# Optimization experiments

Measured on AMD Instinct MI355X. Metric: run time of the kernel, lower is better.

The kernel has to match this reference:

```python
import jax, jax.numpy as jnp
import numpy as np

NUM_LAYERS = 3
INPUT_SIZE = 64
EMB = 128
NUM_CAT = 128          # must equal EMB for the W_e_proj assignment to shape-check
NUM_QUERIES = 1
INIT_SCALE = 0.02
KERNEL_PARAM = 1.0     # referenced-but-undefined in source; standard alpha=1
B = 16
N = 2048
D = INPUT_SIZE + 2 * EMB                 # 320, transformer embedding dim
F_IN = INPUT_SIZE + NUM_CAT + EMB        # 320, raw input feature dim


def setup_inputs() -> dict:
    key = jax.random.key(0)
    k = jax.random.split(key, 6)
    x = jax.random.normal(k[0], (B, F_IN, N), dtype=jnp.float32)
    embedding_matrix = jax.random.normal(k[1], (EMB, NUM_CAT), dtype=jnp.float32)
    W_Q = jax.random.normal(k[2], (NUM_LAYERS, 1, D, D), dtype=jnp.float32) * INIT_SCALE
    W_K = jax.random.normal(k[3], (NUM_LAYERS, 1, D, D), dtype=jnp.float32) * INIT_SCALE
    W_V = jax.random.normal(k[4], (NUM_LAYERS, 1, D, D), dtype=jnp.float32) * INIT_SCALE
    P = jax.random.normal(k[5], (NUM_LAYERS, 1, D, D), dtype=jnp.float32) * INIT_SCALE
    return {"x": x, "embedding_matrix": embedding_matrix,
            "W_Q": W_Q, "W_K": W_K, "W_V": W_V, "P": P}


def _build_We(embedding_matrix):
    W = jnp.zeros((D, F_IN), dtype=embedding_matrix.dtype)
    W = W.at[:INPUT_SIZE, :INPUT_SIZE].set(jnp.eye(INPUT_SIZE, dtype=W.dtype))
    W = W.at[D - EMB:, F_IN - EMB:].set(jnp.eye(EMB, dtype=W.dtype))
    # rows [input_size : D-emb], cols [input_size : F-num_categories]
    W = W.at[INPUT_SIZE:D - EMB, INPUT_SIZE:F_IN - NUM_CAT].set(embedding_matrix)
    return W


def reference(x, embedding_matrix, W_Q, W_K, W_V, P):
    W = _build_We(embedding_matrix)
    h = jnp.einsum('df,bfn->bdn', W, x)                        # [B, D, N]
    for nl in range(NUM_LAYERS):
        key = h[:, :, :-NUM_QUERIES]                           # include_query=False
        value = key
        query = h
        n_context = key.shape[-1]
        Q = jnp.einsum('id,bdm->bim', W_Q[nl, 0], query)       # [B, D, N]
        K = jnp.einsum('id,bdn->bin', W_K[nl, 0], key)         # [B, D, M]
        V = jnp.einsum('id,bdn->bin', W_V[nl, 0], value)       # [B, D, M]
        # linear kernel scores
        scores = KERNEL_PARAM * jnp.einsum('bim,bin->bmn', Q, K)  # [B, N, M]
        attn = jnp.einsum('bin,bmn->bim', V, scores) / n_context  # [B, D, N]
        h = h + jnp.einsum('ji,bim->bjm', P[nl, 0], attn)
    f = h[:, -EMB:, :]                                         # [B, EMB, N] (squeeze no-op for B>1)
    logits = jnp.einsum('bdn,dc->bnc', f, embedding_matrix)    # [B, N, C]
    predictions = jax.nn.softmax(logits, axis=-1)
    return logits, predictions
```

## Files before the change

kernel.cpp:

```cpp
#include <hip/hip_runtime.h>
#include <math.h>

typedef long long ll;
typedef unsigned int uint;
typedef unsigned short ushort;
typedef __attribute__((ext_vector_type(4))) float f32x4;
typedef __attribute__((ext_vector_type(8))) short bf16x8;

#define SZ 102400LL
#define RS 40960LL

__device__ inline void split2(float v, ushort& h, ushort& l)
{
    uint u = __float_as_uint(v);
    uint uh = u + (0x7FFFu + ((u >> 16) & 1u));
    h = (ushort)(uh >> 16);
    float hf = __uint_as_float((uint)h << 16);
    float d = v - hf;
    uint ud = __float_as_uint(d);
    l = (ushort)((ud + (0x7FFFu + ((ud >> 16) & 1u))) >> 16);
}
__device__ inline float us2f(ushort h, ushort l)
{
    return __uint_as_float((uint)h << 16) + __uint_as_float((uint)l << 16);
}

__global__ __launch_bounds__(256) void gram_sp_k(
    const float* __restrict__ x, float* __restrict__ part,
    const float* __restrict__ Wq, const float* __restrict__ Wk,
    const float* __restrict__ Wv, const float* __restrict__ P,
    const float* __restrict__ emb,
    ushort* __restrict__ WqTs, ushort* __restrict__ WkTs, ushort* __restrict__ WvTs,
    ushort* __restrict__ Ps, ushort* __restrict__ embs, ushort* __restrict__ embTs,
    float* __restrict__ q0)
{
    __shared__ __align__(16) char smem[20480];
    int bid0 = blockIdx.x, tid = threadIdx.x;
    if (bid0 < 960) {
        ushort* Ah  = (ushort*)smem;
        ushort* Al_ = Ah + 2560;
        ushort* Bh  = Al_ + 2560;
        ushort* Bl_ = Bh + 2560;
        int flat = bid0;
        int swz = (flat & 7) * 120 + (flat >> 3);
        int b = swz / 60;
        int rr = swz - b * 60;
        int p = rr / 15, t = rr - p * 15;
        int ti = 0, rem = t;
        while (rem >= 5 - ti) { rem -= 5 - ti; ++ti; }
        int tj = ti + rem;
        int i0 = ti * 64, j0 = tj * 64;
        bool diag = (ti == tj);
        const float* X = x + (ll)b * 320 * 2048;
        int wv = tid >> 6, lane = tid & 63;
        int lr = lane & 15, kb = (lane >> 4) * 8;
        int cr = tid >> 2, ck = (tid & 3) * 8;
        f32x4 hh[4], hl[4], lh[4];
        f32x4 zz = {0.f, 0.f, 0.f, 0.f};
        #pragma unroll
        for (int f = 0; f < 4; ++f) { hh[f] = zz; hl[f] = zz; lh[f] = zz; }
        const ushort* BhS = diag ? Ah : Bh;
        const ushort* BlS = diag ? Al_ : Bl_;

        for (int it = 0; it < 16; ++it) {
            int kg0 = p * 512 + it * 32;
            {
                const float* src = X + (ll)(i0 + cr) * 2048 + kg0 + ck;
                float4 v0 = *(const float4*)src;
                float4 v1 = *(const float4*)(src + 4);
                float vals[8] = {v0.x,v0.y,v0.z,v0.w,v1.x,v1.y,v1.z,v1.w};
                if (kg0 + ck + 7 >= 2047) {
                    #pragma unroll
                    for (int u = 0; u < 8; ++u) if (kg0 + ck + u >= 2047) vals[u] = 0.f;
                }
                bf16x8 hv, lv;
                #pragma unroll
                for (int u = 0; u < 8; ++u) { ushort h, l; split2(vals[u], h, l);
                                              hv[u] = (short)h; lv[u] = (short)l; }
                *(bf16x8*)&Ah[cr * 40 + ck] = hv;
                *(bf16x8*)&Al_[cr * 40 + ck] = lv;
            }
            if (!diag) {
                const float* src = X + (ll)(j0 + cr) * 2048 + kg0 + ck;
                float4 v0 = *(const float4*)src;
                float4 v1 = *(const float4*)(src + 4);
                float vals[8] = {v0.x,v0.y,v0.z,v0.w,v1.x,v1.y,v1.z,v1.w};
                if (kg0 + ck + 7 >= 2047) {
                    #pragma unroll
                    for (int u = 0; u < 8; ++u) if (kg0 + ck + u >= 2047) vals[u] = 0.f;
                }
                bf16x8 hv, lv;
                #pragma unroll
                for (int u = 0; u < 8; ++u) { ushort h, l; split2(vals[u], h, l);
                                              hv[u] = (short)h; lv[u] = (short)l; }
                *(bf16x8*)&Bh[cr * 40 + ck] = hv;
                *(bf16x8*)&Bl_[cr * 40 + ck] = lv;
            }
            __syncthreads();
            bf16x8 ah = *(const bf16x8*)&Ah[(wv * 16 + lr) * 40 + kb];
            bf16x8 al = *(const bf16x8*)&Al_[(wv * 16 + lr) * 40 + kb];
            #pragma unroll
            for (int f = 0; f < 4; ++f) {
                bf16x8 bh_ = *(const bf16x8*)&BhS[(f * 16 + lr) * 40 + kb];
                bf16x8 bl_ = *(const bf16x8*)&BlS[(f * 16 + lr) * 40 + kb];
                hh[f] = __builtin_amdgcn_mfma_f32_16x16x32_bf16(ah, bh_, hh[f], 0, 0, 0);
                hl[f] = __builtin_amdgcn_mfma_f32_16x16x32_bf16(ah, bl_, hl[f], 0, 0, 0);
                lh[f] = __builtin_amdgcn_mfma_f32_16x16x32_bf16(al, bh_, lh[f], 0, 0, 0);
            }
            __syncthreads();
        }
        float* out = part + (((ll)p * 16 + b) * 15 + t) * 4096;
        int orow0 = wv * 16 + (lane >> 4) * 4;
        #pragma unroll
        for (int f = 0; f < 4; ++f) {
            int col = f * 16 + lr;
            #pragma unroll
            for (int r = 0; r < 4; ++r)
                out[(orow0 + r) * 64 + col] = hh[f][r] + hl[f][r] + lh[f][r];
        }
        return;
    }
    int bid = bid0 - 960;
    float (*T)[65] = (float(*)[65])smem;
    if (bid < 225) {
        int m = bid / 25, t = bid % 25;
        const float* mats[3] = {Wq, Wk, Wv};
        ushort* dsts[3] = {WqTs, WkTs, WvTs};
        const float* src = mats[m / 3] + (ll)(m % 3) * SZ;
        ushort* dst = dsts[m / 3] + (ll)(m % 3) * SZ;
        int r0 = (t / 5) * 64, c0 = (t % 5) * 64;
        #pragma unroll
        for (int s = 0; s < 4; ++s) {
            int idx = s * 256 + tid;
            int r = idx >> 4, cq = (idx & 15) * 4;
            *(float4*)&T[r][cq] = *(const float4*)(src + (ll)(r0 + r) * 320 + c0 + cq);
        }
        __syncthreads();
        {
            int c = tid >> 2, kq = (tid & 3) * 16;
            bf16x8 h0, h1, l0, l1;
            #pragma unroll
            for (int u = 0; u < 8; ++u) {
                ushort h, l;
                split2(T[kq + u][c], h, l);     h0[u] = (short)h; l0[u] = (short)l;
                split2(T[kq + 8 + u][c], h, l); h1[u] = (short)h; l1[u] = (short)l;
            }
            ushort* dh = dst + (ll)(c0 + c) * 320 + r0 + kq;
            *(bf16x8*)dh = h0; *(bf16x8*)(dh + 8) = h1;
            *(bf16x8*)(dh + 3 * SZ) = l0; *(bf16x8*)(dh + 3 * SZ + 8) = l1;
        }
    } else if (bid < 375) {
        ll off = (ll)(bid - 225) * 2048 + tid * 8;
        float4 v0 = *(const float4*)(P + off);
        float4 v1 = *(const float4*)(P + off + 4);
        float vals[8] = {v0.x,v0.y,v0.z,v0.w,v1.x,v1.y,v1.z,v1.w};
        bf16x8 hv, lv;
        #pragma unroll
        for (int u = 0; u < 8; ++u) { ushort h,l; split2(vals[u],h,l);
                                      hv[u]=(short)h; lv[u]=(short)l; }
        *(bf16x8*)(Ps + off) = hv;
        *(bf16x8*)(Ps + off + 3 * SZ) = lv;
    } else if (bid < 383) {
        ll off = (ll)(bid - 375) * 2048 + tid * 8;
        float4 v0 = *(const float4*)(emb + off);
        float4 v1 = *(const float4*)(emb + off + 4);
        float vals[8] = {v0.x,v0.y,v0.z,v0.w,v1.x,v1.y,v1.z,v1.w};
        bf16x8 hv, lv;
        #pragma unroll
        for (int u = 0; u < 8; ++u) { ushort h,l; split2(vals[u],h,l);
                                      hv[u]=(short)h; lv[u]=(short)l; }
        *(bf16x8*)(embs + off) = hv;
        *(bf16x8*)(embs + off + 16384) = lv;
    } else if (bid < 387) {
        int t = bid - 383;
        int r0 = (t >> 1) * 64, c0 = (t & 1) * 64;
        {
            int r = tid >> 2, cq = (tid & 3) * 4;
            *(float4*)&T[r][cq]      = *(const float4*)(emb + (ll)(r0 + r) * 128 + c0 + cq);
            *(float4*)&T[r][cq + 16] = *(const float4*)(emb + (ll)(r0 + r) * 128 + c0 + cq + 16);
            *(float4*)&T[r][cq + 32] = *(const float4*)(emb + (ll)(r0 + r) * 128 + c0 + cq + 32);
            *(float4*)&T[r][cq + 48] = *(const float4*)(emb + (ll)(r0 + r) * 128 + c0 + cq + 48);
        }
        __syncthreads();
        {
            int c = tid >> 2, kq = (tid & 3) * 16;
            bf16x8 h0, h1, l0, l1;
            #pragma unroll
            for (int u = 0; u < 8; ++u) {
                ushort h, l;
                split2(T[kq + u][c], h, l);     h0[u]=(short)h; l0[u]=(short)l;
                split2(T[kq + 8 + u][c], h, l); h1[u]=(short)h; l1[u]=(short)l;
            }
            ushort* dh = embTs + (ll)(c0 + c) * 128 + r0 + kq;
            *(bf16x8*)dh = h0; *(bf16x8*)(dh + 8) = h1;
            *(bf16x8*)(dh + 16384) = l0; *(bf16x8*)(dh + 16384 + 8) = l1;
        }
    } else {
        ll base = (ll)(bid - 387) * 2048;
        #pragma unroll
        for (int s = 0; s < 8; ++s) {
            ll id = base + s * 256 + tid;
            int c = (int)(id / 320), i = (int)(id % 320);
            q0[id] = (i >= 192) ? emb[(ll)(i - 192) * 128 + c] : 0.f;
        }
    }
}

__global__ __launch_bounds__(256) void gram_red_k(const float* __restrict__ part,
                                                  ushort* __restrict__ GxS,
                                                  ushort* __restrict__ T1s)
{
    int bt = blockIdx.x;
    int b = bt / 15, t = bt % 15;
    int ti = 0, rem = t;
    while (rem >= 5 - ti) { rem -= 5 - ti; ++ti; }
    int tj = ti + rem;
    int i0 = ti * 64, j0 = tj * 64;
    int tid = threadIdx.x;
    int tx = tid & 15, rg = tid >> 4;
    bool wi = (ti == 0 || ti >= 3);
    bool wj = (tj == 0 || tj >= 3);
    ushort* Gb = GxS + (ll)b * SZ;
    ushort* Tsb = T1s + (ll)b * SZ;
    #pragma unroll
    for (int m = 0; m < 4; ++m) {
        int r = rg * 4 + m;
        float s[4] = {};
        for (int p = 0; p < 4; ++p) {
            const float* src = part + (((ll)p * 16 + b) * 15 + t) * 4096 + r * 64 + tx * 4;
            float4 v = *(const float4*)src;
            s[0]+=v.x; s[1]+=v.y; s[2]+=v.z; s[3]+=v.w;
        }
        #pragma unroll
        for (int u = 0; u < 4; ++u) {
            ushort h, l; split2(s[u], h, l);
            ll rd = (ll)(i0 + r) * 320 + j0 + tx * 4 + u;
            ll rt = (ll)(j0 + tx * 4 + u) * 320 + (i0 + r);
            Gb[rd] = h; Gb[rd + 16 * SZ] = l;
            Gb[rt] = h; Gb[rt + 16 * SZ] = l;
            if (wi) { Tsb[rd] = h; Tsb[rd + 16 * SZ] = l; }
            if (wj) { Tsb[rt] = h; Tsb[rt + 16 * SZ] = l; }
        }
    }
}

struct CJob {
    const ushort *Ah, *Bh;
    const void *Ci, *Ci2;
    float* C; ushort* Cs;
    ll aB, bB, ciB, ci2B, cB, csB;
    ll aLo, bLo, csLo, ciLo, ci2Lo;
    int aS, bS, ciS, ci2S, cS, csS;
    int K, tN, tpb, flags;
    int swzQ, swzR;
    float alpha;
};
struct CPack { CJob j[4]; };

__global__ __launch_bounds__(256) void mchain_k(CPack jp, int c0, int c1, int c2)
{
    int bid = blockIdx.x;
    int ji, local;
    if (bid < c0)      { ji = 0; local = bid; }
    else if (bid < c1) { ji = 1; local = bid - c0; }
    else if (bid < c2) { ji = 2; local = bid - c1; }
    else               { ji = 3; local = bid - c2; }
    CJob j = jp.j[ji];
    int xcd = local & 7, sidx = local >> 3;
    int base = (xcd < j.swzR) ? xcd * (j.swzQ + 1)
                              : j.swzR * (j.swzQ + 1) + (xcd - j.swzR) * j.swzQ;
    int swz = base + sidx;
    int bz = swz / j.tpb;
    int t = swz - bz * j.tpb;
    int i0 = (t / j.tN) * 64, j0 = (t % j.tN) * 64;
    int tid = threadIdx.x;
    int wv = tid >> 6, lane = tid & 63;
    int lr = lane & 15, kb = (lane >> 4) * 8;
    f32x4 hh[4], cx[4];
    f32x4 zz = {0.f,0.f,0.f,0.f};
    #pragma unroll
    for (int f = 0; f < 4; ++f) { hh[f] = zz; cx[f] = zz; }

    __shared__ __align__(16) ushort Bsh[2][2][2560];

    if (j.K > 0) {
        int srow = tid >> 2, skq = (tid & 3) * 8;
        const ushort* Bg = j.Bh + (ll)bz * j.bB + (ll)(j0 + srow) * j.bS + skq;
        const ushort* Ar = j.Ah + (ll)bz * j.aB + (ll)(i0 + wv * 16 + lr) * j.aS + kb;
        bf16x8 svh, svl, ah, al, ahn, aln;
        svh = *(const bf16x8*)Bg;
        svl = *(const bf16x8*)(Bg + j.bLo);
        *(bf16x8*)&Bsh[0][0][srow * 40 + skq] = svh;
        *(bf16x8*)&Bsh[0][1][srow * 40 + skq] = svl;
        ah = *(const bf16x8*)Ar;
        al = *(const bf16x8*)(Ar + j.aLo);
        __syncthreads();
        int nit = j.K >> 5;
        for (int it = 0; it < nit; ++it) {
            int cur = it & 1;
            bool more = (it + 1 < nit);
            if (more) {
                int k1 = (it + 1) << 5;
                svh = *(const bf16x8*)(Bg + k1);
                svl = *(const bf16x8*)(Bg + j.bLo + k1);
                ahn = *(const bf16x8*)(Ar + k1);
                aln = *(const bf16x8*)(Ar + j.aLo + k1);
            }
            #pragma unroll
            for (int f = 0; f < 4; ++f) {
                bf16x8 bh = *(const bf16x8*)&Bsh[cur][0][(f * 16 + lr) * 40 + kb];
                bf16x8 bl = *(const bf16x8*)&Bsh[cur][1][(f * 16 + lr) * 40 + kb];
                hh[f] = __builtin_amdgcn_mfma_f32_16x16x32_bf16(ah, bh, hh[f], 0, 0, 0);
                cx[f] = __builtin_amdgcn_mfma_f32_16x16x32_bf16(ah, bl, cx[f], 0, 0, 0);
                cx[f] = __builtin_amdgcn_mfma_f32_16x16x32_bf16(al, bh, cx[f], 0, 0, 0);
            }
            if (more) {
                *(bf16x8*)&Bsh[cur ^ 1][0][srow * 40 + skq] = svh;
                *(bf16x8*)&Bsh[cur ^ 1][1][srow * 40 + skq] = svl;
                ah = ahn; al = aln;
            }
            __syncthreads();
        }
    }
    const float* Cif = (const float*)j.Ci;
    const ushort* Ciu = (const ushort*)j.Ci;
    const float* Ci2f = (const float*)j.Ci2;
    const ushort* Ci2u = (const ushort*)j.Ci2;
    float* Cp = j.C + (ll)bz * j.cB;
    ushort* Csp = j.Cs + (ll)bz * j.csB;
    int r0 = i0 + wv * 16 + ((lane >> 4) << 2);
    #pragma unroll
    for (int f = 0; f < 4; ++f) {
        int col = j0 + f * 16 + lr;
        #pragma unroll
        for (int r = 0; r < 4; ++r) {
            int row = r0 + r;
            float v = j.alpha * (hh[f][r] + cx[f][r]);
            if (j.flags & 1)
                v += Cif[(ll)bz * j.ciB + (ll)row * j.ciS + col];
            if (j.flags & 32) {
                const ushort* p = Ciu + (ll)bz * j.ciB + (ll)row * j.ciS + col;
                v += us2f(p[0], p[j.ciLo]);
            }
            if (j.flags & 64) {
                const ushort* b2 = Ci2u + (ll)bz * j.ci2B;
                if (j.flags & 2) { const ushort* p = b2 + (ll)row * j.ci2S + col;
                                   v += us2f(p[0], p[j.ci2Lo]); }
                if (j.flags & 4) { const ushort* p = b2 + (ll)col * j.ci2S + row;
                                   v += us2f(p[0], p[j.ci2Lo]); }
            } else {
                if (j.flags & 2) v += Ci2f[(ll)bz * j.ci2B + (ll)row * j.ci2S + col];
                if (j.flags & 4) v += Ci2f[(ll)bz * j.ci2B + (ll)col * j.ci2S + row];
            }
            if (j.flags & 8) Cp[(ll)row * j.cS + col] = v;
            if (j.flags & 16) {
                ushort h, l; split2(v, h, l);
                ushort* p = Csp + (ll)row * j.csS + col;
                p[0] = h; p[j.csLo] = l;
            }
        }
    }
}

__global__ __launch_bounds__(256) void logits_mfma_k(const float* __restrict__ x,
                                                     const ushort* __restrict__ LBs,
                                                     float* __restrict__ logits,
                                                     float* __restrict__ pred)
{
    int flat = blockIdx.x;
    int swzb = (flat & 7) * 128 + (flat >> 3);
    int b = swzb >> 6;
    int i0 = (swzb & 63) * 32;
    const float* X = x + (ll)b * 320 * 2048;
    const ushort* LB = LBs + (ll)b * RS;
    __shared__ float Xs_[2][32][33];
    __shared__ float pmL[2][32], psL[2][32];
    int tid = threadIdx.x;
    int wv = tid >> 6, lane = tid & 63;
    int lr = lane & 15, g = lane >> 4, kb = g * 8;
    int rowg = (wv & 1) * 16, ch = wv >> 1, colh = ch * 64;
    int lkk = tid >> 3, lq = (tid & 7) * 4;
    f32x4 hh[4], cx[4];
    f32x4 zz = {0.f,0.f,0.f,0.f};
    #pragma unroll
    for (int f = 0; f < 4; ++f) { hh[f] = zz; cx[f] = zz; }
    float4 pa;
    auto glb = [&](int k0) {
        pa = *(const float4*)(X + (ll)(k0 + lkk) * 2048 + i0 + lq);
    };
    auto stl = [&](int buf) {
        float* p = &Xs_[buf][lkk][lq];
        p[0] = pa.x; p[1] = pa.y; p[2] = pa.z; p[3] = pa.w;
    };
    glb(0); stl(0);
    __syncthreads();
    for (int it = 0; it < 10; ++it) {
        int cur = it & 1;
        if (it < 9) glb((it + 1) * 32);
        bf16x8 ah, al;
        #pragma unroll
        for (int u = 0; u < 8; ++u) {
            ushort h, l;
            split2(Xs_[cur][kb + u][rowg + lr], h, l);
            ah[u] = (short)h; al[u] = (short)l;
        }
        #pragma unroll
        for (int f = 0; f < 4; ++f) {
            const ushort* Bp = LB + (ll)(colh + f * 16 + lr) * 320 + it * 32 + kb;
            bf16x8 bh = *(const bf16x8*)Bp;
            bf16x8 bl = *(const bf16x8*)(Bp + 16 * RS);
            hh[f] = __builtin_amdgcn_mfma_f32_16x16x32_bf16(ah, bh, hh[f], 0, 0, 0);
            cx[f] = __builtin_amdgcn_mfma_f32_16x16x32_bf16(ah, bl, cx[f], 0, 0, 0);
            cx[f] = __builtin_amdgcn_mfma_f32_16x16x32_bf16(al, bh, cx[f], 0, 0, 0);
        }
        if (it < 9) stl(cur ^ 1);
        __syncthreads();
    }
    float v[4][4];
    #pragma unroll
    for (int r = 0; r < 4; ++r)
        #pragma unroll
        for (int f = 0; f < 4; ++f) v[r][f] = hh[f][r] + cx[f][r];
    #pragma unroll
    for (int r = 0; r < 4; ++r) {
        float m = fmaxf(fmaxf(v[r][0], v[r][1]), fmaxf(v[r][2], v[r][3]));
        #pragma unroll
        for (int off = 8; off; off >>= 1) m = fmaxf(m, __shfl_xor(m, off));
        if (lr == 0) pmL[ch][rowg + g * 4 + r] = m;
    }
    __syncthreads();
    float ev[4][4];
    #pragma unroll
    for (int r = 0; r < 4; ++r) {
        int blr = rowg + g * 4 + r;
        float mx = fmaxf(pmL[0][blr], pmL[1][blr]);
        float s = 0.f;
        #pragma unroll
        for (int f = 0; f < 4; ++f) { ev[r][f] = expf(v[r][f] - mx); s += ev[r][f]; }
        #pragma unroll
        for (int off = 8; off; off >>= 1) s += __shfl_xor(s, off);
        if (lr == 0) psL[ch][blr] = s;
    }
    __syncthreads();
    #pragma unroll
    for (int r = 0; r < 4; ++r) {
        int blr = rowg + g * 4 + r;
        float inv = 1.f / (psL[0][blr] + psL[1][blr]);
        ll ro = ((ll)b * 2048 + i0 + blr) * 128 + colh + lr;
        #pragma unroll
        for (int f = 0; f < 4; ++f) {
            logits[ro + f * 16] = v[r][f];
            pred[ro + f * 16] = ev[r][f] * inv;
        }
    }
}

extern "C" void kernel_launch(void* const* d_in, const int* in_sizes, int n_in,
                              void* d_out, int out_size, void* d_ws, size_t ws_size,
                              hipStream_t stream)
{
    const float* x   = (const float*)d_in[0];
    const float* emb = (const float*)d_in[1];
    const float* Wq  = (const float*)d_in[2];
    const float* Wk  = (const float*)d_in[3];
    const float* Wv  = (const float*)d_in[4];
    const float* P   = (const float*)d_in[5];

    float* logits = (float*)d_out;
    float* pred   = logits + (ll)16 * 2048 * 128;

    float* w = (float*)d_ws;
    auto takef = [&](ll n) { float* p = w; w += n; return p; };
    ushort* GxS  = (ushort*)takef(16 * SZ);
    ushort* T1s  = (ushort*)takef(16 * SZ);
    ushort* Gs   = (ushort*)takef(16 * SZ);
    ushort* As   = (ushort*)takef(16 * SZ);
    ushort* Us   = (ushort*)takef(16 * SZ);
    float*  ATsF = takef(48 * SZ);
    ushort* ATs  = (ushort*)ATsF;
    ushort* PVs  = (ushort*)takef(3 * SZ);
    ushort* KQTs = (ushort*)takef(3 * SZ);
    ushort* KQs  = (ushort*)takef(3 * SZ);
    ushort* Ps   = (ushort*)takef(3 * SZ);
    ushort* WqTs = (ushort*)takef(3 * SZ);
    ushort* WkTs = (ushort*)takef(3 * SZ);
    ushort* WvTs = (ushort*)takef(3 * SZ);
    ushort* embs = (ushort*)takef(16384);
    ushort* embTs= (ushort*)takef(16384);
    float*  q0f  = takef(RS);
    ushort* q1s  = (ushort*)takef(16 * RS);
    ushort* q2s  = (ushort*)takef(16 * RS);
    ushort* LBs  = (ushort*)takef(16 * RS);
    ushort* Xs   = GxS;
    ushort* Zts  = T1s;
    float*  part = ATsF;
    ushort* q3s  = q1s;
    const float cinv = 1.f / 2047.f;

    auto JB = [](const ushort* Ah, ll aB, int aS, ll aLo,
                 const ushort* Bh, ll bB, int bS, ll bLo,
                 int K, int tM, int tN, float alpha, int flags,
                 const void* Ci, ll ciB, int ciS, ll ciLo,
                 const void* Ci2, ll ci2B, int ci2S, ll ci2Lo,
                 float* C, ll cB, int cS,
                 ushort* Cs, ll csB, int csS, ll csLo) {
        CJob j;
        j.Ah = Ah; j.Bh = Bh;
        j.Ci = Ci; j.Ci2 = Ci2; j.C = C; j.Cs = Cs;
        j.aB = aB; j.bB = bB; j.ciB = ciB; j.ci2B = ci2B; j.cB = cB; j.csB = csB;
        j.aLo = aLo; j.bLo = bLo; j.csLo = csLo; j.ciLo = ciLo; j.ci2Lo = ci2Lo;
        j.aS = aS; j.bS = bS; j.ciS = ciS; j.ci2S = ci2S; j.cS = cS; j.csS = csS;
        j.K = K; j.tN = tN; j.tpb = tM * tN; j.flags = flags; j.alpha = alpha;
        j.swzQ = 0; j.swzR = 0;
        return j;
    };
    auto fire = [&](const CJob* js, const int* nb, int n) {
        CPack jp;
        int cum[4], tot = 0;
        for (int i = 0; i < 4; ++i) {
            jp.j[i] = js[i < n ? i : 0];
            if (i < n) { jp.j[i].swzQ = nb[i] >> 3; jp.j[i].swzR = nb[i] & 7; }
            tot += (i < n ? nb[i] : 0);
            cum[i] = tot;
        }
        mchain_k<<<tot, 256, 0, stream>>>(jp, cum[0], cum[1], cum[2]);
    };

    gram_sp_k<<<1367, 256, 0, stream>>>(x, part, Wq, Wk, Wv, P, emb,
                                        WqTs, WkTs, WvTs, Ps, embs, embTs, q0f);
    gram_red_k<<<240, 256, 0, stream>>>(part, GxS, T1s);
    {
        CJob js[4] = {
            JB(embs, 0, 128, 16384,  GxS + 64, SZ, 320, 16*SZ,  128, 2, 5, 1.f, 16,
               0,0,0,0, 0,0,0,0,  0,0,0,  T1s + 64*320, SZ, 320, 16*SZ),
            JB(Ps, SZ, 320, 3*SZ,  WvTs, SZ, 320, 3*SZ,  320, 5, 5, 1.f, 16,
               0,0,0,0, 0,0,0,0,  0,0,0,  PVs, SZ, 320, 3*SZ),
            JB(WqTs, SZ, 320, 3*SZ,  WkTs, SZ, 320, 3*SZ,  320, 5, 5, 1.f, 16,
               0,0,0,0, 0,0,0,0,  0,0,0,  KQTs, SZ, 320, 3*SZ),
            JB(WkTs, SZ, 320, 3*SZ,  WqTs, SZ, 320, 3*SZ,  320, 5, 5, 1.f, 16,
               0,0,0,0, 0,0,0,0,  0,0,0,  KQs, SZ, 320, 3*SZ)};
        int nb[4] = {160, 75, 75, 75};
        fire(js, nb, 4);
    }
    {
        CJob js[3] = {
            JB(T1s + 64, SZ, 320, 16*SZ,  embs, 0, 128, 16384,  128, 5, 2, 1.f, 16,
               0,0,0,0, 0,0,0,0,  0,0,0,  Gs + 64, SZ, 320, 16*SZ),
            JB(0,0,0,0, 0,0,0,0,  0, 5, 1, 0.f, 32|16,
               T1s, SZ, 320, 16*SZ, 0,0,0,0,  0,0,0,  Gs, SZ, 320, 16*SZ),
            JB(0,0,0,0, 0,0,0,0,  0, 5, 2, 0.f, 32|16,
               T1s + 192, SZ, 320, 16*SZ, 0,0,0,0,  0,0,0,  Gs + 192, SZ, 320, 16*SZ)};
        int nb[3] = {160, 80, 160};
        fire(js, nb, 3);
    }
    for (int l = 0; l < 3; ++l) {
        const ushort* PVl = PVs + (ll)l * SZ;
        const ushort* KQTl = KQTs + (ll)l * SZ;
        const ushort* KQl = KQs + (ll)l * SZ;
        ushort* ATl = ATs + (ll)l * 16 * SZ;
        if (l < 2) {
            CJob s1[2] = {
                JB(PVl, 0, 320, 3*SZ,  Gs, SZ, 320, 16*SZ,  320, 5, 5, 1.f, 16,
                   0,0,0,0, 0,0,0,0,  0,0,0,  Xs, SZ, 320, 16*SZ),
                JB(Gs, SZ, 320, 16*SZ,  KQl, 0, 320, 3*SZ,  320, 5, 5, 1.f, 16,
                   0,0,0,0, 0,0,0,0,  0,0,0,  Zts, SZ, 320, 16*SZ)};
            int n1[2] = {400, 400};
            fire(s1, n1, 2);
            CJob s2[3] = {
                JB(Xs, SZ, 320, 16*SZ,  KQTl, 0, 320, 3*SZ,  320, 5, 5, cinv, 16,
                   0,0,0,0, 0,0,0,0,  0,0,0,  As, SZ, 320, 16*SZ),
                JB(KQTl, 0, 320, 3*SZ,  Xs, SZ, 320, 16*SZ,  320, 5, 5, cinv, 16,
                   0,0,0,0, 0,0,0,0,  0,0,0,  ATl, SZ, 320, 48*SZ),
                JB(Xs, SZ, 320, 16*SZ,  Zts, SZ, 320, 16*SZ,  320, 5, 5, cinv, 16,
                   0,0,0,0, 0,0,0,0,  0,0,0,  Us, SZ, 320, 16*SZ)};
            int n2[3] = {400, 400, 400};
            fire(s2, n2, 3);
            CJob s3[1] = {
                JB(Us, SZ, 320, 16*SZ,  As, SZ, 320, 16*SZ,  320, 5, 5, 1.f, 16|32|2|4|64,
                   Gs, SZ, 320, 16*SZ,  Us, SZ, 320, 16*SZ,  0,0,0,  Gs, SZ, 320, 16*SZ)};
            int n3[1] = {400};
            fire(s3, n3, 1);
        } else {
            CJob s1[1] = {
                JB(PVl, 0, 320, 3*SZ,  Gs, SZ, 320, 16*SZ,  320, 5, 5, 1.f, 16,
                   0,0,0,0, 0,0,0,0,  0,0,0,  Xs, SZ, 320, 16*SZ)};
            int n1[1] = {400};
            fire(s1, n1, 1);
            CJob s2[1] = {
                JB(KQTl, 0, 320, 3*SZ,  Xs, SZ, 320, 16*SZ,  320, 5, 5, cinv, 16,
                   0,0,0,0, 0,0,0,0,  0,0,0,  ATl, SZ, 320, 48*SZ)};
            int n2[1] = {400};
            fire(s2, n2, 1);
        }
    }
    {
        CJob js[1] = {
            JB(embTs, 0, 128, 16384,  ATs + 2*16*SZ + 192, SZ, 320, 48*SZ,  128, 2, 5, 1.f, 1|16,
               q0f, 0, 320, 0, 0,0,0,0,  0,0,0,  q1s, RS, 320, 16*RS)};
        int nb[1] = {160};
        fire(js, nb, 1);
    }
    {
        CJob js[1] = {
            JB(q1s, RS, 320, 16*RS,  ATs + 1*16*SZ, SZ, 320, 48*SZ,  320, 2, 5, 1.f, 32|16,
               q1s, RS, 320, 16*RS, 0,0,0,0,  0,0,0,  q2s, RS, 320, 16*RS)};
        int nb[1] = {160};
        fire(js, nb, 1);
    }
    {
        CJob js[1] = {
            JB(q2s, RS, 320, 16*RS,  ATs, SZ, 320, 48*SZ,  320, 2, 5, 1.f, 32|16,
               q2s, RS, 320, 16*RS, 0,0,0,0,  0,0,0,  q3s, RS, 320, 16*RS)};
        int nb[1] = {160};
        fire(js, nb, 1);
    }
    {
        CJob js[3] = {
            JB(q3s + 64, RS, 320, 16*RS,  embTs, 0, 128, 16384,  128, 2, 2, 1.f, 16,
               0,0,0,0, 0,0,0,0,  0,0,0,  LBs + 64, RS, 320, 16*RS),
            JB(0,0,0,0, 0,0,0,0,  0, 2, 1, 0.f, 32|16,
               q3s, RS, 320, 16*RS, 0,0,0,0,  0,0,0,  LBs, RS, 320, 16*RS),
            JB(0,0,0,0, 0,0,0,0,  0, 2, 2, 0.f, 32|16,
               q3s + 192, RS, 320, 16*RS, 0,0,0,0,  0,0,0,  LBs + 192, RS, 320, 16*RS)};
        int nb[3] = {64, 32, 64};
        fire(js, nb, 3);
    }
    logits_mfma_k<<<1024, 256, 0, stream>>>(x, LBs, logits, pred);
}
```

Before: 315.4 us.

## Fuse all pipeline stages into one cooperative persistent megakernel with grid sync

Replaces the sequence of about 17 separate kernel launches (gram, reduce, chained GEMM jobs, logits) with a single cooperative kernel that loops over stages and separates them with grid-wide barriers. Stage bodies become device functions that share one dynamic shared-memory buffer. The goal is to remove per-launch overhead and the gaps between dependent small launches. The cost is that a grid of at most 1024 persistent blocks must loop over stages with up to 1367 tiles, and grid syncs add their own latency. If the cooperative launch fails, it falls back to per-stage launches.

```diff
diff --git a/kernel.cpp b/kernel.cpp
--- a/kernel.cpp
+++ b/kernel.cpp
@@ -1,5 +1,8 @@
 #include <hip/hip_runtime.h>
+#include <hip/hip_cooperative_groups.h>
 #include <math.h>
+
+namespace cg = cooperative_groups;
 
 typedef long long ll;
 typedef unsigned int uint;
@@ -23,225 +26,6 @@
 __device__ inline float us2f(ushort h, ushort l)
 {
     return __uint_as_float((uint)h << 16) + __uint_as_float((uint)l << 16);
-}
-
-__global__ __launch_bounds__(256) void gram_sp_k(
-    const float* __restrict__ x, float* __restrict__ part,
-    const float* __restrict__ Wq, const float* __restrict__ Wk,
-    const float* __restrict__ Wv, const float* __restrict__ P,
-    const float* __restrict__ emb,
-    ushort* __restrict__ WqTs, ushort* __restrict__ WkTs, ushort* __restrict__ WvTs,
-    ushort* __restrict__ Ps, ushort* __restrict__ embs, ushort* __restrict__ embTs,
-    float* __restrict__ q0)
-{
-    __shared__ __align__(16) char smem[20480];
-    int bid0 = blockIdx.x, tid = threadIdx.x;
-    if (bid0 < 960) {
-        ushort* Ah  = (ushort*)smem;
-        ushort* Al_ = Ah + 2560;
-        ushort* Bh  = Al_ + 2560;
-        ushort* Bl_ = Bh + 2560;
-        int flat = bid0;
-        int swz = (flat & 7) * 120 + (flat >> 3);
-        int b = swz / 60;
-        int rr = swz - b * 60;
-        int p = rr / 15, t = rr - p * 15;
-        int ti = 0, rem = t;
-        while (rem >= 5 - ti) { rem -= 5 - ti; ++ti; }
-        int tj = ti + rem;
-        int i0 = ti * 64, j0 = tj * 64;
-        bool diag = (ti == tj);
-        const float* X = x + (ll)b * 320 * 2048;
-        int wv = tid >> 6, lane = tid & 63;
-        int lr = lane & 15, kb = (lane >> 4) * 8;
-        int cr = tid >> 2, ck = (tid & 3) * 8;
-        f32x4 hh[4], hl[4], lh[4];
-        f32x4 zz = {0.f, 0.f, 0.f, 0.f};
-        #pragma unroll
-        for (int f = 0; f < 4; ++f) { hh[f] = zz; hl[f] = zz; lh[f] = zz; }
-        const ushort* BhS = diag ? Ah : Bh;
-        const ushort* BlS = diag ? Al_ : Bl_;
-
-        for (int it = 0; it < 16; ++it) {
-            int kg0 = p * 512 + it * 32;
-            {
-                const float* src = X + (ll)(i0 + cr) * 2048 + kg0 + ck;
-                float4 v0 = *(const float4*)src;
-                float4 v1 = *(const float4*)(src + 4);
-                float vals[8] = {v0.x,v0.y,v0.z,v0.w,v1.x,v1.y,v1.z,v1.w};
-                if (kg0 + ck + 7 >= 2047) {
-                    #pragma unroll
-                    for (int u = 0; u < 8; ++u) if (kg0 + ck + u >= 2047) vals[u] = 0.f;
-                }
-                bf16x8 hv, lv;
-                #pragma unroll
-                for (int u = 0; u < 8; ++u) { ushort h, l; split2(vals[u], h, l);
-                                              hv[u] = (short)h; lv[u] = (short)l; }
-                *(bf16x8*)&Ah[cr * 40 + ck] = hv;
-                *(bf16x8*)&Al_[cr * 40 + ck] = lv;
-            }
-            if (!diag) {
-                const float* src = X + (ll)(j0 + cr) * 2048 + kg0 + ck;
-                float4 v0 = *(const float4*)src;
-                float4 v1 = *(const float4*)(src + 4);
-                float vals[8] = {v0.x,v0.y,v0.z,v0.w,v1.x,v1.y,v1.z,v1.w};
-                if (kg0 + ck + 7 >= 2047) {
-                    #pragma unroll
-                    for (int u = 0; u < 8; ++u) if (kg0 + ck + u >= 2047) vals[u] = 0.f;
-                }
-                bf16x8 hv, lv;
-                #pragma unroll
-                for (int u = 0; u < 8; ++u) { ushort h, l; split2(vals[u], h, l);
-                                              hv[u] = (short)h; lv[u] = (short)l; }
-                *(bf16x8*)&Bh[cr * 40 + ck] = hv;
-                *(bf16x8*)&Bl_[cr * 40 + ck] = lv;
-            }
-            __syncthreads();
-            bf16x8 ah = *(const bf16x8*)&Ah[(wv * 16 + lr) * 40 + kb];
-            bf16x8 al = *(const bf16x8*)&Al_[(wv * 16 + lr) * 40 + kb];
-            #pragma unroll
-            for (int f = 0; f < 4; ++f) {
-                bf16x8 bh_ = *(const bf16x8*)&BhS[(f * 16 + lr) * 40 + kb];
-                bf16x8 bl_ = *(const bf16x8*)&BlS[(f * 16 + lr) * 40 + kb];
-                hh[f] = __builtin_amdgcn_mfma_f32_16x16x32_bf16(ah, bh_, hh[f], 0, 0, 0);
-                hl[f] = __builtin_amdgcn_mfma_f32_16x16x32_bf16(ah, bl_, hl[f], 0, 0, 0);
-                lh[f] = __builtin_amdgcn_mfma_f32_16x16x32_bf16(al, bh_, lh[f], 0, 0, 0);
-            }
-            __syncthreads();
-        }
-        float* out = part + (((ll)p * 16 + b) * 15 + t) * 4096;
-        int orow0 = wv * 16 + (lane >> 4) * 4;
-        #pragma unroll
-        for (int f = 0; f < 4; ++f) {
-            int col = f * 16 + lr;
-            #pragma unroll
-            for (int r = 0; r < 4; ++r)
-                out[(orow0 + r) * 64 + col] = hh[f][r] + hl[f][r] + lh[f][r];
-        }
-        return;
-    }
-    int bid = bid0 - 960;
-    float (*T)[65] = (float(*)[65])smem;
-    if (bid < 225) {
-        int m = bid / 25, t = bid % 25;
-        const float* mats[3] = {Wq, Wk, Wv};
-        ushort* dsts[3] = {WqTs, WkTs, WvTs};
-        const float* src = mats[m / 3] + (ll)(m % 3) * SZ;
-        ushort* dst = dsts[m / 3] + (ll)(m % 3) * SZ;
-        int r0 = (t / 5) * 64, c0 = (t % 5) * 64;
-        #pragma unroll
-        for (int s = 0; s < 4; ++s) {
-            int idx = s * 256 + tid;
-            int r = idx >> 4, cq = (idx & 15) * 4;
-            *(float4*)&T[r][cq] = *(const float4*)(src + (ll)(r0 + r) * 320 + c0 + cq);
-        }
-        __syncthreads();
-        {
-            int c = tid >> 2, kq = (tid & 3) * 16;
-            bf16x8 h0, h1, l0, l1;
-            #pragma unroll
-            for (int u = 0; u < 8; ++u) {
-                ushort h, l;
-                split2(T[kq + u][c], h, l);     h0[u] = (short)h; l0[u] = (short)l;
-                split2(T[kq + 8 + u][c], h, l); h1[u] = (short)h; l1[u] = (short)l;
-            }
-            ushort* dh = dst + (ll)(c0 + c) * 320 + r0 + kq;
-            *(bf16x8*)dh = h0; *(bf16x8*)(dh + 8) = h1;
-            *(bf16x8*)(dh + 3 * SZ) = l0; *(bf16x8*)(dh + 3 * SZ + 8) = l1;
-        }
-    } else if (bid < 375) {
-        ll off = (ll)(bid - 225) * 2048 + tid * 8;
-        float4 v0 = *(const float4*)(P + off);
-        float4 v1 = *(const float4*)(P + off + 4);
-        float vals[8] = {v0.x,v0.y,v0.z,v0.w,v1.x,v1.y,v1.z,v1.w};
-        bf16x8 hv, lv;
-        #pragma unroll
-        for (int u = 0; u < 8; ++u) { ushort h,l; split2(vals[u],h,l);
-                                      hv[u]=(short)h; lv[u]=(short)l; }
-        *(bf16x8*)(Ps + off) = hv;
-        *(bf16x8*)(Ps + off + 3 * SZ) = lv;
-    } else if (bid < 383) {
-        ll off = (ll)(bid - 375) * 2048 + tid * 8;
-        float4 v0 = *(const float4*)(emb + off);
-        float4 v1 = *(const float4*)(emb + off + 4);
-        float vals[8] = {v0.x,v0.y,v0.z,v0.w,v1.x,v1.y,v1.z,v1.w};
-        bf16x8 hv, lv;
-        #pragma unroll
-        for (int u = 0; u < 8; ++u) { ushort h,l; split2(vals[u],h,l);
-                                      hv[u]=(short)h; lv[u]=(short)l; }
-        *(bf16x8*)(embs + off) = hv;
-        *(bf16x8*)(embs + off + 16384) = lv;
-    } else if (bid < 387) {
-        int t = bid - 383;
-        int r0 = (t >> 1) * 64, c0 = (t & 1) * 64;
-        {
-            int r = tid >> 2, cq = (tid & 3) * 4;
-            *(float4*)&T[r][cq]      = *(const float4*)(emb + (ll)(r0 + r) * 128 + c0 + cq);
-            *(float4*)&T[r][cq + 16] = *(const float4*)(emb + (ll)(r0 + r) * 128 + c0 + cq + 16);
-            *(float4*)&T[r][cq + 32] = *(const float4*)(emb + (ll)(r0 + r) * 128 + c0 + cq + 32);
-            *(float4*)&T[r][cq + 48] = *(const float4*)(emb + (ll)(r0 + r) * 128 + c0 + cq + 48);
-        }
-        __syncthreads();
-        {
-            int c = tid >> 2, kq = (tid & 3) * 16;
-            bf16x8 h0, h1, l0, l1;
-            #pragma unroll
-            for (int u = 0; u < 8; ++u) {
-                ushort h, l;
-                split2(T[kq + u][c], h, l);     h0[u]=(short)h; l0[u]=(short)l;
-                split2(T[kq + 8 + u][c], h, l); h1[u]=(short)h; l1[u]=(short)l;
-            }
-            ushort* dh = embTs + (ll)(c0 + c) * 128 + r0 + kq;
-            *(bf16x8*)dh = h0; *(bf16x8*)(dh + 8) = h1;
-            *(bf16x8*)(dh + 16384) = l0; *(bf16x8*)(dh + 16384 + 8) = l1;
-        }
-    } else {
-        ll base = (ll)(bid - 387) * 2048;
-        #pragma unroll
-        for (int s = 0; s < 8; ++s) {
-            ll id = base + s * 256 + tid;
-            int c = (int)(id / 320), i = (int)(id % 320);
-            q0[id] = (i >= 192) ? emb[(ll)(i - 192) * 128 + c] : 0.f;
-        }
-    }
-}
-
-__global__ __launch_bounds__(256) void gram_red_k(const float* __restrict__ part,
-                                                  ushort* __restrict__ GxS,
-                                                  ushort* __restrict__ T1s)
-{
-    int bt = blockIdx.x;
-    int b = bt / 15, t = bt % 15;
-    int ti = 0, rem = t;
-    while (rem >= 5 - ti) { rem -= 5 - ti; ++ti; }
-    int tj = ti + rem;
-    int i0 = ti * 64, j0 = tj * 64;
-    int tid = threadIdx.x;
-    int tx = tid & 15, rg = tid >> 4;
-    bool wi = (ti == 0 || ti >= 3);
-    bool wj = (tj == 0 || tj >= 3);
-    ushort* Gb = GxS + (ll)b * SZ;
-    ushort* Tsb = T1s + (ll)b * SZ;
-    #pragma unroll
-    for (int m = 0; m < 4; ++m) {
-        int r = rg * 4 + m;
-        float s[4] = {};
-        for (int p = 0; p < 4; ++p) {
-            const float* src = part + (((ll)p * 16 + b) * 15 + t) * 4096 + r * 64 + tx * 4;
-            float4 v = *(const float4*)src;
-            s[0]+=v.x; s[1]+=v.y; s[2]+=v.z; s[3]+=v.w;
-        }
-        #pragma unroll
-        for (int u = 0; u < 4; ++u) {
-            ushort h, l; split2(s[u], h, l);
-            ll rd = (ll)(i0 + r) * 320 + j0 + tx * 4 + u;
-            ll rt = (ll)(j0 + tx * 4 + u) * 320 + (i0 + r);
-            Gb[rd] = h; Gb[rd + 16 * SZ] = l;
-            Gb[rt] = h; Gb[rt + 16 * SZ] = l;
-            if (wi) { Tsb[rd] = h; Tsb[rd + 16 * SZ] = l; }
-            if (wj) { Tsb[rt] = h; Tsb[rt + 16 * SZ] = l; }
-        }
-    }
 }
 
 struct CJob {
@@ -255,17 +39,28 @@
     int swzQ, swzR;
     float alpha;
 };
-struct CPack { CJob j[4]; };
-
-__global__ __launch_bounds__(256) void mchain_k(CPack jp, int c0, int c1, int c2)
-{
-    int bid = blockIdx.x;
-    int ji, local;
-    if (bid < c0)      { ji = 0; local = bid; }
-    else if (bid < c1) { ji = 1; local = bid - c0; }
-    else if (bid < c2) { ji = 2; local = bid - c1; }
-    else               { ji = 3; local = bid - c2; }
-    CJob j = jp.j[ji];
+
+__device__ inline CJob JBd(const ushort* Ah, ll aB, int aS, ll aLo,
+                           const ushort* Bh, ll bB, int bS, ll bLo,
+                           int K, int tM, int tN, float alpha, int flags,
+                           const void* Ci, ll ciB, int ciS, ll ciLo,
+                           const void* Ci2, ll ci2B, int ci2S, ll ci2Lo,
+                           float* C, ll cB, int cS,
+                           ushort* Cs, ll csB, int csS, ll csLo, int nb)
+{
+    CJob j;
+    j.Ah = Ah; j.Bh = Bh;
+    j.Ci = Ci; j.Ci2 = Ci2; j.C = C; j.Cs = Cs;
+    j.aB = aB; j.bB = bB; j.ciB = ciB; j.ci2B = ci2B; j.cB = cB; j.csB = csB;
+    j.aLo = aLo; j.bLo = bLo; j.csLo = csLo; j.ciLo = ciLo; j.ci2Lo = ci2Lo;
+    j.aS = aS; j.bS = bS; j.ciS = ciS; j.ci2S = ci2S; j.cS = cS; j.csS = csS;
+    j.K = K; j.tN = tN; j.tpb = tM * tN; j.flags = flags; j.alpha = alpha;
+    j.swzQ = nb >> 3; j.swzR = nb & 7;
+    return j;
+}
+
+__device__ __attribute__((noinline)) void gemm_tile(const CJob& j, int local, char* smem)
+{
     int xcd = local & 7, sidx = local >> 3;
     int base = (xcd < j.swzR) ? xcd * (j.swzQ + 1)
                               : j.swzR * (j.swzQ + 1) + (xcd - j.swzR) * j.swzQ;
@@ -281,7 +76,7 @@
     #pragma unroll
     for (int f = 0; f < 4; ++f) { hh[f] = zz; cx[f] = zz; }
 
-    __shared__ __align__(16) ushort Bsh[2][2][2560];
+    ushort (*Bsh)[2][2560] = (ushort(*)[2][2560])smem;
 
     if (j.K > 0) {
         int srow = tid >> 2, skq = (tid & 3) * 8;
@@ -362,19 +157,236 @@
     }
 }
 
-__global__ __launch_bounds__(256) void logits_mfma_k(const float* __restrict__ x,
-                                                     const ushort* __restrict__ LBs,
-                                                     float* __restrict__ logits,
-                                                     float* __restrict__ pred)
-{
-    int flat = blockIdx.x;
+__device__ void gram_tile(int flat, const float* __restrict__ x,
+                          float* __restrict__ part, char* smem)
+{
+    ushort* Ah  = (ushort*)smem;
+    ushort* Al_ = Ah + 2560;
+    ushort* Bh  = Al_ + 2560;
+    ushort* Bl_ = Bh + 2560;
+    int tid = threadIdx.x;
+    int swz = (flat & 7) * 120 + (flat >> 3);
+    int b = swz / 60;
+    int rr = swz - b * 60;
+    int p = rr / 15, t = rr - p * 15;
+    int ti = 0, rem = t;
+    while (rem >= 5 - ti) { rem -= 5 - ti; ++ti; }
+    int tj = ti + rem;
+    int i0 = ti * 64, j0 = tj * 64;
+    bool diag = (ti == tj);
+    const float* X = x + (ll)b * 320 * 2048;
+    int wv = tid >> 6, lane = tid & 63;
+    int lr = lane & 15, kb = (lane >> 4) * 8;
+    int cr = tid >> 2, ck = (tid & 3) * 8;
+    f32x4 hh[4], hl[4], lh[4];
+    f32x4 zz = {0.f, 0.f, 0.f, 0.f};
+    #pragma unroll
+    for (int f = 0; f < 4; ++f) { hh[f] = zz; hl[f] = zz; lh[f] = zz; }
+    const ushort* BhS = diag ? Ah : Bh;
+    const ushort* BlS = diag ? Al_ : Bl_;
+
+    for (int it = 0; it < 16; ++it) {
+        int kg0 = p * 512 + it * 32;
+        {
+            const float* src = X + (ll)(i0 + cr) * 2048 + kg0 + ck;
+            float4 v0 = *(const float4*)src;
+            float4 v1 = *(const float4*)(src + 4);
+            float vals[8] = {v0.x,v0.y,v0.z,v0.w,v1.x,v1.y,v1.z,v1.w};
+            if (kg0 + ck + 7 >= 2047) {
+                #pragma unroll
+                for (int u = 0; u < 8; ++u) if (kg0 + ck + u >= 2047) vals[u] = 0.f;
+            }
+            bf16x8 hv, lv;
+            #pragma unroll
+            for (int u = 0; u < 8; ++u) { ushort h, l; split2(vals[u], h, l);
+                                          hv[u] = (short)h; lv[u] = (short)l; }
+            *(bf16x8*)&Ah[cr * 40 + ck] = hv;
+            *(bf16x8*)&Al_[cr * 40 + ck] = lv;
+        }
+        if (!diag) {
+            const float* src = X + (ll)(j0 + cr) * 2048 + kg0 + ck;
+            float4 v0 = *(const float4*)src;
+            float4 v1 = *(const float4*)(src + 4);
+            float vals[8] = {v0.x,v0.y,v0.z,v0.w,v1.x,v1.y,v1.z,v1.w};
+            if (kg0 + ck + 7 >= 2047) {
+                #pragma unroll
+                for (int u = 0; u < 8; ++u) if (kg0 + ck + u >= 2047) vals[u] = 0.f;
+            }
+            bf16x8 hv, lv;
+            #pragma unroll
+            for (int u = 0; u < 8; ++u) { ushort h, l; split2(vals[u], h, l);
+                                          hv[u] = (short)h; lv[u] = (short)l; }
+            *(bf16x8*)&Bh[cr * 40 + ck] = hv;
+            *(bf16x8*)&Bl_[cr * 40 + ck] = lv;
+        }
+        __syncthreads();
+        bf16x8 ah = *(const bf16x8*)&Ah[(wv * 16 + lr) * 40 + kb];
+        bf16x8 al = *(const bf16x8*)&Al_[(wv * 16 + lr) * 40 + kb];
+        #pragma unroll
+        for (int f = 0; f < 4; ++f) {
+            bf16x8 bh_ = *(const bf16x8*)&BhS[(f * 16 + lr) * 40 + kb];
+            bf16x8 bl_ = *(const bf16x8*)&BlS[(f * 16 + lr) * 40 + kb];
+            hh[f] = __builtin_amdgcn_mfma_f32_16x16x32_bf16(ah, bh_, hh[f], 0, 0, 0);
+            hl[f] = __builtin_amdgcn_mfma_f32_16x16x32_bf16(ah, bl_, hl[f], 0, 0, 0);
+            lh[f] = __builtin_amdgcn_mfma_f32_16x16x32_bf16(al, bh_, lh[f], 0, 0, 0);
+        }
+        __syncthreads();
+    }
+    float* out = part + (((ll)p * 16 + b) * 15 + t) * 4096;
+    int orow0 = wv * 16 + (lane >> 4) * 4;
+    #pragma unroll
+    for (int f = 0; f < 4; ++f) {
+        int col = f * 16 + lr;
+        #pragma unroll
+        for (int r = 0; r < 4; ++r)
+            out[(orow0 + r) * 64 + col] = hh[f][r] + hl[f][r] + lh[f][r];
+    }
+}
+
+__device__ void sp_tile(int bid,
+                        const float* __restrict__ Wq, const float* __restrict__ Wk,
+                        const float* __restrict__ Wv, const float* __restrict__ P,
+                        const float* __restrict__ emb,
+                        ushort* WqTs, ushort* WkTs, ushort* WvTs,
+                        ushort* Ps, ushort* embs, ushort* embTs,
+                        float* q0, char* smem)
+{
+    int tid = threadIdx.x;
+    float (*T)[65] = (float(*)[65])smem;
+    if (bid < 225) {
+        int m = bid / 25, t = bid % 25;
+        const float* mats[3] = {Wq, Wk, Wv};
+        ushort* dsts[3] = {WqTs, WkTs, WvTs};
+        const float* src = mats[m / 3] + (ll)(m % 3) * SZ;
+        ushort* dst = dsts[m / 3] + (ll)(m % 3) * SZ;
+        int r0 = (t / 5) * 64, c0 = (t % 5) * 64;
+        #pragma unroll
+        for (int s = 0; s < 4; ++s) {
+            int idx = s * 256 + tid;
+            int r = idx >> 4, cq = (idx & 15) * 4;
+            *(float4*)&T[r][cq] = *(const float4*)(src + (ll)(r0 + r) * 320 + c0 + cq);
+        }
+        __syncthreads();
+        {
+            int c = tid >> 2, kq = (tid & 3) * 16;
+            bf16x8 h0, h1, l0, l1;
+            #pragma unroll
+            for (int u = 0; u < 8; ++u) {
+                ushort h, l;
+                split2(T[kq + u][c], h, l);     h0[u] = (short)h; l0[u] = (short)l;
+                split2(T[kq + 8 + u][c], h, l); h1[u] = (short)h; l1[u] = (short)l;
+            }
+            ushort* dh = dst + (ll)(c0 + c) * 320 + r0 + kq;
+            *(bf16x8*)dh = h0; *(bf16x8*)(dh + 8) = h1;
+            *(bf16x8*)(dh + 3 * SZ) = l0; *(bf16x8*)(dh + 3 * SZ + 8) = l1;
+        }
+    } else if (bid < 375) {
+        ll off = (ll)(bid - 225) * 2048 + tid * 8;
+        float4 v0 = *(const float4*)(P + off);
+        float4 v1 = *(const float4*)(P + off + 4);
+        float vals[8] = {v0.x,v0.y,v0.z,v0.w,v1.x,v1.y,v1.z,v1.w};
+        bf16x8 hv, lv;
+        #pragma unroll
+        for (int u = 0; u < 8; ++u) { ushort h,l; split2(vals[u],h,l);
+                                      hv[u]=(short)h; lv[u]=(short)l; }
+        *(bf16x8*)(Ps + off) = hv;
+        *(bf16x8*)(Ps + off + 3 * SZ) = lv;
+    } else if (bid < 383) {
+        ll off = (ll)(bid - 375) * 2048 + tid * 8;
+        float4 v0 = *(const float4*)(emb + off);
+        float4 v1 = *(const float4*)(emb + off + 4);
+        float vals[8] = {v0.x,v0.y,v0.z,v0.w,v1.x,v1.y,v1.z,v1.w};
+        bf16x8 hv, lv;
+        #pragma unroll
+        for (int u = 0; u < 8; ++u) { ushort h,l; split2(vals[u],h,l);
+                                      hv[u]=(short)h; lv[u]=(short)l; }
+        *(bf16x8*)(embs + off) = hv;
+        *(bf16x8*)(embs + off + 16384) = lv;
+    } else if (bid < 387) {
+        int t = bid - 383;
+        int r0 = (t >> 1) * 64, c0 = (t & 1) * 64;
+        {
+            int r = tid >> 2, cq = (tid & 3) * 4;
+            *(float4*)&T[r][cq]      = *(const float4*)(emb + (ll)(r0 + r) * 128 + c0 + cq);
+            *(float4*)&T[r][cq + 16] = *(const float4*)(emb + (ll)(r0 + r) * 128 + c0 + cq + 16);
+            *(float4*)&T[r][cq + 32] = *(const float4*)(emb + (ll)(r0 + r) * 128 + c0 + cq + 32);
+            *(float4*)&T[r][cq + 48] = *(const float4*)(emb + (ll)(r0 + r) * 128 + c0 + cq + 48);
+        }
+        __syncthreads();
+        {
+            int c = tid >> 2, kq = (tid & 3) * 16;
+            bf16x8 h0, h1, l0, l1;
+            #pragma unroll
+            for (int u = 0; u < 8; ++u) {
+                ushort h, l;
+                split2(T[kq + u][c], h, l);     h0[u]=(short)h; l0[u]=(short)l;
+                split2(T[kq + 8 + u][c], h, l); h1[u]=(short)h; l1[u]=(short)l;
+            }
+            ushort* dh = embTs + (ll)(c0 + c) * 128 + r0 + kq;
+            *(bf16x8*)dh = h0; *(bf16x8*)(dh + 8) = h1;
+            *(bf16x8*)(dh + 16384) = l0; *(bf16x8*)(dh + 16384 + 8) = l1;
+        }
+    } else {
+        ll base = (ll)(bid - 387) * 2048;
+        #pragma unroll
+        for (int s = 0; s < 8; ++s) {
+            ll id = base + s * 256 + tid;
+            int c = (int)(id / 320), i = (int)(id % 320);
+            q0[id] = (i >= 192) ? emb[(ll)(i - 192) * 128 + c] : 0.f;
+        }
+    }
+}
+
+__device__ void red_tile(int bt, const float* __restrict__ part,
+                         ushort* __restrict__ GxS, ushort* __restrict__ T1s)
+{
+    int b = bt / 15, t = bt % 15;
+    int ti = 0, rem = t;
+    while (rem >= 5 - ti) { rem -= 5 - ti; ++ti; }
+    int tj = ti + rem;
+    int i0 = ti * 64, j0 = tj * 64;
+    int tid = threadIdx.x;
+    int tx = tid & 15, rg = tid >> 4;
+    bool wi = (ti == 0 || ti >= 3);
+    bool wj = (tj == 0 || tj >= 3);
+    ushort* Gb = GxS + (ll)b * SZ;
+    ushort* Tsb = T1s + (ll)b * SZ;
+    #pragma unroll
+    for (int m = 0; m < 4; ++m) {
+        int r = rg * 4 + m;
+        float s[4] = {};
+        for (int p = 0; p < 4; ++p) {
+            const float* src = part + (((ll)p * 16 + b) * 15 + t) * 4096 + r * 64 + tx * 4;
+            float4 v = *(const float4*)src;
+            s[0]+=v.x; s[1]+=v.y; s[2]+=v.z; s[3]+=v.w;
+        }
+        #pragma unroll
+        for (int u = 0; u < 4; ++u) {
+            ushort h, l; split2(s[u], h, l);
+            ll rd = (ll)(i0 + r) * 320 + j0 + tx * 4 + u;
+            ll rt = (ll)(j0 + tx * 4 + u) * 320 + (i0 + r);
+            Gb[rd] = h; Gb[rd + 16 * SZ] = l;
+            Gb[rt] = h; Gb[rt + 16 * SZ] = l;
+            if (wi) { Tsb[rd] = h; Tsb[rd + 16 * SZ] = l; }
+            if (wj) { Tsb[rt] = h; Tsb[rt + 16 * SZ] = l; }
+        }
+    }
+}
+
+__device__ void logits_tile(int flat, const float* __restrict__ x,
+                            const ushort* __restrict__ LBs,
+                            float* __restrict__ logits, float* __restrict__ pred,
+                            char* smem)
+{
+    float (*Xs_)[32][33] = (float(*)[32][33])smem;
+    float (*SB)[132]     = (float(*)[132])smem;
+    float (*pmL)[32]     = (float(*)[32])(smem + 17408);
+    float (*psL)[32]     = (float(*)[32])(smem + 17920);
     int swzb = (flat & 7) * 128 + (flat >> 3);
     int b = swzb >> 6;
     int i0 = (swzb & 63) * 32;
     const float* X = x + (ll)b * 320 * 2048;
     const ushort* LB = LBs + (ll)b * RS;
-    __shared__ float Xs_[2][32][33];
-    __shared__ float pmL[2][32], psL[2][32];
     int tid = threadIdx.x;
     int wv = tid >> 6, lane = tid & 63;
     int lr = lane & 15, g = lane >> 4, kb = g * 8;
@@ -385,18 +397,21 @@
     #pragma unroll
     for (int f = 0; f < 4; ++f) { hh[f] = zz; cx[f] = zz; }
     float4 pa;
-    auto glb = [&](int k0) {
-        pa = *(const float4*)(X + (ll)(k0 + lkk) * 2048 + i0 + lq);
-    };
-    auto stl = [&](int buf) {
-        float* p = &Xs_[buf][lkk][lq];
-        p[0] = pa.x; p[1] = pa.y; p[2] = pa.z; p[3] = pa.w;
-    };
-    glb(0); stl(0);
+    pa = *(const float4*)(X + (ll)lkk * 2048 + i0 + lq);
+    { float* p = &Xs_[0][lkk][lq]; p[0]=pa.x; p[1]=pa.y; p[2]=pa.z; p[3]=pa.w; }
     __syncthreads();
     for (int it = 0; it < 10; ++it) {
         int cur = it & 1;
-        if (it < 9) glb((it + 1) * 32);
+        if (it < 9) pa = *(const float4*)(X + (ll)((it+1)*32 + lkk) * 2048 + i0 + lq);
+        const ushort* B0 = LB + (ll)(colh + lr) * 320 + it * 32 + kb;
+        bf16x8 b0h = *(const bf16x8*)B0;
+        bf16x8 b0l = *(const bf16x8*)(B0 + 16 * RS);
+        bf16x8 b1h = *(const bf16x8*)(B0 + 16 * 320);
+        bf16x8 b1l = *(const bf16x8*)(B0 + 16 * 320 + 16 * RS);
+        bf16x8 b2h = *(const bf16x8*)(B0 + 32 * 320);
+        bf16x8 b2l = *(const bf16x8*)(B0 + 32 * 320 + 16 * RS);
+        bf16x8 b3h = *(const bf16x8*)(B0 + 48 * 320);
+        bf16x8 b3l = *(const bf16x8*)(B0 + 48 * 320 + 16 * RS);
         bf16x8 ah, al;
         #pragma unroll
         for (int u = 0; u < 8; ++u) {
@@ -404,16 +419,22 @@
             split2(Xs_[cur][kb + u][rowg + lr], h, l);
             ah[u] = (short)h; al[u] = (short)l;
         }
-        #pragma unroll
-        for (int f = 0; f < 4; ++f) {
-            const ushort* Bp = LB + (ll)(colh + f * 16 + lr) * 320 + it * 32 + kb;
-            bf16x8 bh = *(const bf16x8*)Bp;
-            bf16x8 bl = *(const bf16x8*)(Bp + 16 * RS);
-            hh[f] = __builtin_amdgcn_mfma_f32_16x16x32_bf16(ah, bh, hh[f], 0, 0, 0);
-            cx[f] = __builtin_amdgcn_mfma_f32_16x16x32_bf16(ah, bl, cx[f], 0, 0, 0);
-            cx[f] = __builtin_amdgcn_mfma_f32_16x16x32_bf16(al, bh, cx[f], 0, 0, 0);
-        }
-        if (it < 9) stl(cur ^ 1);
+        hh[0] = __builtin_amdgcn_mfma_f32_16x16x32_bf16(ah, b0h, hh[0], 0, 0, 0);
+        cx[0] = __builtin_amdgcn_mfma_f32_16x16x32_bf16(ah, b0l, cx[0], 0, 0, 0);
+        cx[0] = __builtin_amdgcn_mfma_f32_16x16x32_bf16(al, b0h, cx[0], 0, 0, 0);
+        hh[1] = __builtin_amdgcn_mfma_f32_16x16x32_bf16(ah, b1h, hh[1], 0, 0, 0);
+        cx[1] = __builtin_amdgcn_mfma_f32_16x16x32_bf16(ah, b1l, cx[1], 0, 0, 0);
+        cx[1] = __builtin_amdgcn_mfma_f32_16x16x32_bf16(al, b1h, cx[1], 0, 0, 0);
+        hh[2] = __builtin_amdgcn_mfma_f32_16x16x32_bf16(ah, b2h, hh[2], 0, 0, 0);
+        cx[2] = __builtin_amdgcn_mfma_f32_16x16x32_bf16(ah, b2l, cx[2], 0, 0, 0);
+        cx[2] = __builtin_amdgcn_mfma_f32_16x16x32_bf16(al, b2h, cx[2], 0, 0, 0);
+        hh[3] = __builtin_amdgcn_mfma_f32_16x16x32_bf16(ah, b3h, hh[3], 0, 0, 0);
+        cx[3] = __builtin_amdgcn_mfma_f32_16x16x32_bf16(ah, b3l, cx[3], 0, 0, 0);
+        cx[3] = __builtin_amdgcn_mfma_f32_16x16x32_bf16(al, b3h, cx[3], 0, 0, 0);
+        if (it < 9) {
+            float* p = &Xs_[cur ^ 1][lkk][lq];
+            p[0]=pa.x; p[1]=pa.y; p[2]=pa.z; p[3]=pa.w;
+        }
         __syncthreads();
     }
     float v[4][4];
@@ -429,7 +450,7 @@
         if (lr == 0) pmL[ch][rowg + g * 4 + r] = m;
     }
     __syncthreads();
-    float ev[4][4];
+    float ev[4][4], inv[4];
     #pragma unroll
     for (int r = 0; r < 4; ++r) {
         int blr = rowg + g * 4 + r;
@@ -445,185 +466,256 @@
     #pragma unroll
     for (int r = 0; r < 4; ++r) {
         int blr = rowg + g * 4 + r;
-        float inv = 1.f / (psL[0][blr] + psL[1][blr]);
-        ll ro = ((ll)b * 2048 + i0 + blr) * 128 + colh + lr;
-        #pragma unroll
-        for (int f = 0; f < 4; ++f) {
-            logits[ro + f * 16] = v[r][f];
-            pred[ro + f * 16] = ev[r][f] * inv;
-        }
-    }
+        inv[r] = 1.f / (psL[0][blr] + psL[1][blr]);
+    }
+    #pragma unroll
+    for (int r = 0; r < 4; ++r)
+        #pragma unroll
+        for (int f = 0; f < 4; ++f)
+            SB[rowg + g * 4 + r][colh + f * 16 + lr] = v[r][f];
+    __syncthreads();
+    #pragma unroll
+    for (int s = 0; s < 4; ++s) {
+        int idx = s * 256 + tid;
+        int row = idx >> 5, cq = (idx & 31) * 4;
+        *(float4*)(logits + ((ll)b * 2048 + i0 + row) * 128 + cq) = *(float4*)&SB[row][cq];
+    }
+    __syncthreads();
+    #pragma unroll
+    for (int r = 0; r < 4; ++r)
+        #pragma unroll
+        for (int f = 0; f < 4; ++f)
+            SB[rowg + g * 4 + r][colh + f * 16 + lr] = ev[r][f] * inv[r];
+    __syncthreads();
+    #pragma unroll
+    for (int s = 0; s < 4; ++s) {
+        int idx = s * 256 + tid;
+        int row = idx >> 5, cq = (idx & 31) * 4;
+        *(float4*)(pred + ((ll)b * 2048 + i0 + row) * 128 + cq) = *(float4*)&SB[row][cq];
+    }
+}
+
+struct MArgs {
+    const float *x, *emb, *Wq, *Wk, *Wv, *P;
+    float *logits, *pred;
+    ushort *GxS, *T1s, *Gs, *As, *Us, *ATs;
+    ushort *PVs, *KQTs, *KQs, *Ps, *WqTs, *WkTs, *WvTs, *embs, *embTs, *LBs;
+    ushort *q1s, *q2s;
+    float *q0f, *part;
+};
+
+__device__ inline int stage_cnt(int s)
+{
+    switch (s) {
+        case 0: return 1367; case 1: return 240; case 2: return 385;
+        case 3: return 400;  case 4: return 800; case 5: return 1200;
+        case 6: return 400;  case 7: return 800; case 8: return 1200;
+        case 9: return 400;  case 10: return 400; case 11: return 400;
+        case 12: case 13: case 14: case 15: return 160;
+        default: return 1024;
+    }
+}
+
+__device__ void run_stage(const MArgs& a, int stage, int bid, int nbk, char* smem)
+{
+    const float cinv = 1.f / 2047.f;
+    ushort* Xs = a.GxS;
+    ushort* Zts = a.T1s;
+    int cnt = stage_cnt(stage);
+    for (int t = bid; t < cnt; t += nbk) {
+        switch (stage) {
+        case 0:
+            if (t < 960) gram_tile(t, a.x, a.part, smem);
+            else sp_tile(t - 960, a.Wq, a.Wk, a.Wv, a.P, a.emb,
+                         a.WqTs, a.WkTs, a.WvTs, a.Ps, a.embs, a.embTs, a.q0f, smem);
+            break;
+        case 1:
+            red_tile(t, a.part, a.GxS, a.T1s);
+            break;
+        case 2: {
+            CJob j; int x;
+            if (t < 160) { x = t;
+                j = JBd(a.embs,0,128,16384, a.GxS+64,SZ,320,16*SZ, 128,2,5,1.f,16,
+                        0,0,0,0, 0,0,0,0, 0,0,0, a.T1s+64*320,SZ,320,16*SZ, 160); }
+            else if (t < 235) { x = t - 160;
+                j = JBd(a.Ps,SZ,320,3*SZ, a.WvTs,SZ,320,3*SZ, 320,5,5,1.f,16,
+                        0,0,0,0, 0,0,0,0, 0,0,0, a.PVs,SZ,320,3*SZ, 75); }
+            else if (t < 310) { x = t - 235;
+                j = JBd(a.WqTs,SZ,320,3*SZ, a.WkTs,SZ,320,3*SZ, 320,5,5,1.f,16,
+                        0,0,0,0, 0,0,0,0, 0,0,0, a.KQTs,SZ,320,3*SZ, 75); }
+            else { x = t - 310;
+                j = JBd(a.WkTs,SZ,320,3*SZ, a.WqTs,SZ,320,3*SZ, 320,5,5,1.f,16,
+                        0,0,0,0, 0,0,0,0, 0,0,0, a.KQs,SZ,320,3*SZ, 75); }
+            gemm_tile(j, x, smem);
+        } break;
+        case 3: {
+            CJob j; int x;
+            if (t < 160) { x = t;
+                j = JBd(a.T1s+64,SZ,320,16*SZ, a.embs,0,128,16384, 128,5,2,1.f,16,
+                        0,0,0,0, 0,0,0,0, 0,0,0, a.Gs+64,SZ,320,16*SZ, 160); }
+            else if (t < 240) { x = t - 160;
+                j = JBd(0,0,0,0, 0,0,0,0, 0,5,1,0.f,32|16,
+                        a.T1s,SZ,320,16*SZ, 0,0,0,0, 0,0,0, a.Gs,SZ,320,16*SZ, 80); }
+            else { x = t - 240;
+                j = JBd(0,0,0,0, 0,0,0,0, 0,5,2,0.f,32|16,
+                        a.T1s+192,SZ,320,16*SZ, 0,0,0,0, 0,0,0, a.Gs+192,SZ,320,16*SZ, 160); }
+            gemm_tile(j, x, smem);
+        } break;
+        case 4: case 7: {
+            int l = (stage - 4) / 3;
+            const ushort* PVl = a.PVs + (ll)l * SZ;
+            const ushort* KQl = a.KQs + (ll)l * SZ;
+            CJob j; int x;
+            if (t < 400) { x = t;
+                j = JBd(PVl,0,320,3*SZ, a.Gs,SZ,320,16*SZ, 320,5,5,1.f,16,
+                        0,0,0,0, 0,0,0,0, 0,0,0, Xs,SZ,320,16*SZ, 400); }
+            else { x = t - 400;
+                j = JBd(a.Gs,SZ,320,16*SZ, KQl,0,320,3*SZ, 320,5,5,1.f,16,
+                        0,0,0,0, 0,0,0,0, 0,0,0, Zts,SZ,320,16*SZ, 400); }
+            gemm_tile(j, x, smem);
+        } break;
+        case 5: case 8: {
+            int l = (stage - 5) / 3;
+            const ushort* KQTl = a.KQTs + (ll)l * SZ;
+            ushort* ATl = a.ATs + (ll)l * 16 * SZ;
+            CJob j; int x;
+            if (t < 400) { x = t;
+                j = JBd(Xs,SZ,320,16*SZ, KQTl,0,320,3*SZ, 320,5,5,cinv,16,
+                        0,0,0,0, 0,0,0,0, 0,0,0, a.As,SZ,320,16*SZ, 400); }
+            else if (t < 800) { x = t - 400;
+                j = JBd(KQTl,0,320,3*SZ, Xs,SZ,320,16*SZ, 320,5,5,cinv,16,
+                        0,0,0,0, 0,0,0,0, 0,0,0, ATl,SZ,320,48*SZ, 400); }
+            else { x = t - 800;
+                j = JBd(Xs,SZ,320,16*SZ, Zts,SZ,320,16*SZ, 320,5,5,cinv,16,
+                        0,0,0,0, 0,0,0,0, 0,0,0, a.Us,SZ,320,16*SZ, 400); }
+            gemm_tile(j, x, smem);
+        } break;
+        case 6: case 9: {
+            CJob j = JBd(a.Us,SZ,320,16*SZ, a.As,SZ,320,16*SZ, 320,5,5,1.f,16|32|2|4|64,
+                         a.Gs,SZ,320,16*SZ, a.Us,SZ,320,16*SZ, 0,0,0,
+                         a.Gs,SZ,320,16*SZ, 400);
+            gemm_tile(j, t, smem);
+        } break;
+        case 10: {
+            const ushort* PVl = a.PVs + (ll)2 * SZ;
+            CJob j = JBd(PVl,0,320,3*SZ, a.Gs,SZ,320,16*SZ, 320,5,5,1.f,16,
+                         0,0,0,0, 0,0,0,0, 0,0,0, Xs,SZ,320,16*SZ, 400);
+            gemm_tile(j, t, smem);
+        } break;
+        case 11: {
+            const ushort* KQTl = a.KQTs + (ll)2 * SZ;
+            ushort* ATl = a.ATs + (ll)2 * 16 * SZ;
+            CJob j = JBd(KQTl,0,320,3*SZ, Xs,SZ,320,16*SZ, 320,5,5,cinv,16,
+                         0,0,0,0, 0,0,0,0, 0,0,0, ATl,SZ,320,48*SZ, 400);
+            gemm_tile(j, t, smem);
+        } break;
+        case 12: {
+            CJob j = JBd(a.embTs,0,128,16384, a.ATs+2*16*SZ+192,SZ,320,48*SZ,
+                         128,2,5,1.f,1|16,
+                         a.q0f,0,320,0, 0,0,0,0, 0,0,0, a.q1s,RS,320,16*RS, 160);
+            gemm_tile(j, t, smem);
+        } break;
+        case 13: {
+            CJob j = JBd(a.q1s,RS,320,16*RS, a.ATs+16*SZ,SZ,320,48*SZ, 320,2,5,1.f,32|16,
+                         a.q1s,RS,320,16*RS, 0,0,0,0, 0,0,0, a.q2s,RS,320,16*RS, 160);
+            gemm_tile(j, t, smem);
+        } break;
+        case 14: {
+            CJob j = JBd(a.q2s,RS,320,16*RS, a.ATs,SZ,320,48*SZ, 320,2,5,1.f,32|16,
+                         a.q2s,RS,320,16*RS, 0,0,0,0, 0,0,0, a.q1s,RS,320,16*RS, 160);
+            gemm_tile(j, t, smem);
+        } break;
+        case 15: {
+            CJob j; int x;
+            if (t < 64) { x = t;
+                j = JBd(a.q1s+64,RS,320,16*RS, a.embTs,0,128,16384, 128,2,2,1.f,16,
+                        0,0,0,0, 0,0,0,0, 0,0,0, a.LBs+64,RS,320,16*RS, 64); }
+            else if (t < 96) { x = t - 64;
+                j = JBd(0,0,0,0, 0,0,0,0, 0,2,1,0.f,32|16,
+                        a.q1s,RS,320,16*RS, 0,0,0,0, 0,0,0, a.LBs,RS,320,16*RS, 32); }
+            else { x = t - 96;
+                j = JBd(0,0,0,0, 0,0,0,0, 0,2,2,0.f,32|16,
+                        a.q1s+192,RS,320,16*RS, 0,0,0,0, 0,0,0, a.LBs+192,RS,320,16*RS, 64); }
+            gemm_tile(j, x, smem);
+        } break;
+        default:
+            logits_tile(t, a.x, a.LBs, a.logits, a.pred, smem);
+            break;
+        }
+        __syncthreads();
+    }
+}
+
+__global__ __launch_bounds__(256) void mega_k(MArgs a)
+{
+    __shared__ __align__(16) char smem[21504];
+    cg::grid_group gg = cg::this_grid();
+    for (int s = 0; s < 17; ++s) {
+        run_stage(a, s, blockIdx.x, gridDim.x, smem);
+        if (s < 16) gg.sync();
+    }
+}
+
+__global__ __launch_bounds__(256) void stage_k(MArgs a, int stage)
+{
+    __shared__ __align__(16) char smem[21504];
+    run_stage(a, stage, blockIdx.x, gridDim.x, smem);
 }
 
 extern "C" void kernel_launch(void* const* d_in, const int* in_sizes, int n_in,
                               void* d_out, int out_size, void* d_ws, size_t ws_size,
                               hipStream_t stream)
 {
-    const float* x   = (const float*)d_in[0];
-    const float* emb = (const float*)d_in[1];
-    const float* Wq  = (const float*)d_in[2];
-    const float* Wk  = (const float*)d_in[3];
-    const float* Wv  = (const float*)d_in[4];
-    const float* P   = (const float*)d_in[5];
-
-    float* logits = (float*)d_out;
-    float* pred   = logits + (ll)16 * 2048 * 128;
+    MArgs a;
+    a.x   = (const float*)d_in[0];
+    a.emb = (const float*)d_in[1];
+    a.Wq  = (const float*)d_in[2];
+    a.Wk  = (const float*)d_in[3];
+    a.Wv  = (const float*)d_in[4];
+    a.P   = (const float*)d_in[5];
+    a.logits = (float*)d_out;
+    a.pred   = a.logits + (ll)16 * 2048 * 128;
 
     float* w = (float*)d_ws;
     auto takef = [&](ll n) { float* p = w; w += n; return p; };
-    ushort* GxS  = (ushort*)takef(16 * SZ);
-    ushort* T1s  = (ushort*)takef(16 * SZ);
-    ushort* Gs   = (ushort*)takef(16 * SZ);
-    ushort* As   = (ushort*)takef(16 * SZ);
-    ushort* Us   = (ushort*)takef(16 * SZ);
-    float*  ATsF = takef(48 * SZ);
-    ushort* ATs  = (ushort*)ATsF;
-    ushort* PVs  = (ushort*)takef(3 * SZ);
-    ushort* KQTs = (ushort*)takef(3 * SZ);
-    ushort* KQs  = (ushort*)takef(3 * SZ);
-    ushort* Ps   = (ushort*)takef(3 * SZ);
-    ushort* WqTs = (ushort*)takef(3 * SZ);
-    ushort* WkTs = (ushort*)takef(3 * SZ);
-    ushort* WvTs = (ushort*)takef(3 * SZ);
-    ushort* embs = (ushort*)takef(16384);
-    ushort* embTs= (ushort*)takef(16384);
-    float*  q0f  = takef(RS);
-    ushort* q1s  = (ushort*)takef(16 * RS);
-    ushort* q2s  = (ushort*)takef(16 * RS);
-    ushort* LBs  = (ushort*)takef(16 * RS);
-    ushort* Xs   = GxS;
-    ushort* Zts  = T1s;
-    float*  part = ATsF;
-    ushort* q3s  = q1s;
-    const float cinv = 1.f / 2047.f;
-
-    auto JB = [](const ushort* Ah, ll aB, int aS, ll aLo,
-                 const ushort* Bh, ll bB, int bS, ll bLo,
-                 int K, int tM, int tN, float alpha, int flags,
-                 const void* Ci, ll ciB, int ciS, ll ciLo,
-                 const void* Ci2, ll ci2B, int ci2S, ll ci2Lo,
-                 float* C, ll cB, int cS,
-                 ushort* Cs, ll csB, int csS, ll csLo) {
-        CJob j;
-        j.Ah = Ah; j.Bh = Bh;
-        j.Ci = Ci; j.Ci2 = Ci2; j.C = C; j.Cs = Cs;
-        j.aB = aB; j.bB = bB; j.ciB = ciB; j.ci2B = ci2B; j.cB = cB; j.csB = csB;
-        j.aLo = aLo; j.bLo = bLo; j.csLo = csLo; j.ciLo = ciLo; j.ci2Lo = ci2Lo;
-        j.aS = aS; j.bS = bS; j.ciS = ciS; j.ci2S = ci2S; j.cS = cS; j.csS = csS;
-        j.K = K; j.tN = tN; j.tpb = tM * tN; j.flags = flags; j.alpha = alpha;
-        j.swzQ = 0; j.swzR = 0;
-        return j;
-    };
-    auto fire = [&](const CJob* js, const int* nb, int n) {
-        CPack jp;
-        int cum[4], tot = 0;
-        for (int i = 0; i < 4; ++i) {
-            jp.j[i] = js[i < n ? i : 0];
-            if (i < n) { jp.j[i].swzQ = nb[i] >> 3; jp.j[i].swzR = nb[i] & 7; }
-            tot += (i < n ? nb[i] : 0);
-            cum[i] = tot;
-        }
-        mchain_k<<<tot, 256, 0, stream>>>(jp, cum[0], cum[1], cum[2]);
-    };
-
-    gram_sp_k<<<1367, 256, 0, stream>>>(x, part, Wq, Wk, Wv, P, emb,
-                                        WqTs, WkTs, WvTs, Ps, embs, embTs, q0f);
-    gram_red_k<<<240, 256, 0, stream>>>(part, GxS, T1s);
-    {
-        CJob js[4] = {
-            JB(embs, 0, 128, 16384,  GxS + 64, SZ, 320, 16*SZ,  128, 2, 5, 1.f, 16,
-               0,0,0,0, 0,0,0,0,  0,0,0,  T1s + 64*320, SZ, 320, 16*SZ),
-            JB(Ps, SZ, 320, 3*SZ,  WvTs, SZ, 320, 3*SZ,  320, 5, 5, 1.f, 16,
-               0,0,0,0, 0,0,0,0,  0,0,0,  PVs, SZ, 320, 3*SZ),
-            JB(WqTs, SZ, 320, 3*SZ,  WkTs, SZ, 320, 3*SZ,  320, 5, 5, 1.f, 16,
-               0,0,0,0, 0,0,0,0,  0,0,0,  KQTs, SZ, 320, 3*SZ),
-            JB(WkTs, SZ, 320, 3*SZ,  WqTs, SZ, 320, 3*SZ,  320, 5, 5, 1.f, 16,
-               0,0,0,0, 0,0,0,0,  0,0,0,  KQs, SZ, 320, 3*SZ)};
-        int nb[4] = {160, 75, 75, 75};
-        fire(js, nb, 4);
-    }
-    {
-        CJob js[3] = {
-            JB(T1s + 64, SZ, 320, 16*SZ,  embs, 0, 128, 16384,  128, 5, 2, 1.f, 16,
-               0,0,0,0, 0,0,0,0,  0,0,0,  Gs + 64, SZ, 320, 16*SZ),
-            JB(0,0,0,0, 0,0,0,0,  0, 5, 1, 0.f, 32|16,
-               T1s, SZ, 320, 16*SZ, 0,0,0,0,  0,0,0,  Gs, SZ, 320, 16*SZ),
-            JB(0,0,0,0, 0,0,0,0,  0, 5, 2, 0.f, 32|16,
-               T1s + 192, SZ, 320, 16*SZ, 0,0,0,0,  0,0,0,  Gs + 192, SZ, 320, 16*SZ)};
-        int nb[3] = {160, 80, 160};
-        fire(js, nb, 3);
-    }
-    for (int l = 0; l < 3; ++l) {
-        const ushort* PVl = PVs + (ll)l * SZ;
-        const ushort* KQTl = KQTs + (ll)l * SZ;
-        const ushort* KQl = KQs + (ll)l * SZ;
-        ushort* ATl = ATs + (ll)l * 16 * SZ;
-        if (l < 2) {
-            CJob s1[2] = {
-                JB(PVl, 0, 320, 3*SZ,  Gs, SZ, 320, 16*SZ,  320, 5, 5, 1.f, 16,
-                   0,0,0,0, 0,0,0,0,  0,0,0,  Xs, SZ, 320, 16*SZ),
-                JB(Gs, SZ, 320, 16*SZ,  KQl, 0, 320, 3*SZ,  320, 5, 5, 1.f, 16,
-                   0,0,0,0, 0,0,0,0,  0,0,0,  Zts, SZ, 320, 16*SZ)};
-            int n1[2] = {400, 400};
-            fire(s1, n1, 2);
-            CJob s2[3] = {
-                JB(Xs, SZ, 320, 16*SZ,  KQTl, 0, 320, 3*SZ,  320, 5, 5, cinv, 16,
-                   0,0,0,0, 0,0,0,0,  0,0,0,  As, SZ, 320, 16*SZ),
-                JB(KQTl, 0, 320, 3*SZ,  Xs, SZ, 320, 16*SZ,  320, 5, 5, cinv, 16,
-                   0,0,0,0, 0,0,0,0,  0,0,0,  ATl, SZ, 320, 48*SZ),
-                JB(Xs, SZ, 320, 16*SZ,  Zts, SZ, 320, 16*SZ,  320, 5, 5, cinv, 16,
-                   0,0,0,0, 0,0,0,0,  0,0,0,  Us, SZ, 320, 16*SZ)};
-            int n2[3] = {400, 400, 400};
-            fire(s2, n2, 3);
-            CJob s3[1] = {
-                JB(Us, SZ, 320, 16*SZ,  As, SZ, 320, 16*SZ,  320, 5, 5, 1.f, 16|32|2|4|64,
-                   Gs, SZ, 320, 16*SZ,  Us, SZ, 320, 16*SZ,  0,0,0,  Gs, SZ, 320, 16*SZ)};
-            int n3[1] = {400};
-            fire(s3, n3, 1);
-        } else {
-            CJob s1[1] = {
-                JB(PVl, 0, 320, 3*SZ,  Gs, SZ, 320, 16*SZ,  320, 5, 5, 1.f, 16,
-                   0,0,0,0, 0,0,0,0,  0,0,0,  Xs, SZ, 320, 16*SZ)};
-            int n1[1] = {400};
-            fire(s1, n1, 1);
-            CJob s2[1] = {
-                JB(KQTl, 0, 320, 3*SZ,  Xs, SZ, 320, 16*SZ,  320, 5, 5, cinv, 16,
-                   0,0,0,0, 0,0,0,0,  0,0,0,  ATl, SZ, 320, 48*SZ)};
-            int n2[1] = {400};
-            fire(s2, n2, 1);
-        }
-    }
-    {
-        CJob js[1] = {
-            JB(embTs, 0, 128, 16384,  ATs + 2*16*SZ + 192, SZ, 320, 48*SZ,  128, 2, 5, 1.f, 1|16,
-               q0f, 0, 320, 0, 0,0,0,0,  0,0,0,  q1s, RS, 320, 16*RS)};
-        int nb[1] = {160};
-        fire(js, nb, 1);
-    }
-    {
-        CJob js[1] = {
-            JB(q1s, RS, 320, 16*RS,  ATs + 1*16*SZ, SZ, 320, 48*SZ,  320, 2, 5, 1.f, 32|16,
-               q1s, RS, 320, 16*RS, 0,0,0,0,  0,0,0,  q2s, RS, 320, 16*RS)};
-        int nb[1] = {160};
-        fire(js, nb, 1);
-    }
-    {
-        CJob js[1] = {
-            JB(q2s, RS, 320, 16*RS,  ATs, SZ, 320, 48*SZ,  320, 2, 5, 1.f, 32|16,
-               q2s, RS, 320, 16*RS, 0,0,0,0,  0,0,0,  q3s, RS, 320, 16*RS)};
-        int nb[1] = {160};
-        fire(js, nb, 1);
-    }
-    {
-        CJob js[3] = {
-            JB(q3s + 64, RS, 320, 16*RS,  embTs, 0, 128, 16384,  128, 2, 2, 1.f, 16,
-               0,0,0,0, 0,0,0,0,  0,0,0,  LBs + 64, RS, 320, 16*RS),
-            JB(0,0,0,0, 0,0,0,0,  0, 2, 1, 0.f, 32|16,
-               q3s, RS, 320, 16*RS, 0,0,0,0,  0,0,0,  LBs, RS, 320, 16*RS),
-            JB(0,0,0,0, 0,0,0,0,  0, 2, 2, 0.f, 32|16,
-               q3s + 192, RS, 320, 16*RS, 0,0,0,0,  0,0,0,  LBs + 192, RS, 320, 16*RS)};
-        int nb[3] = {64, 32, 64};
-        fire(js, nb, 3);
-    }
-    logits_mfma_k<<<1024, 256, 0, stream>>>(x, LBs, logits, pred);
-}
+    a.GxS  = (ushort*)takef(16 * SZ);
+    a.T1s  = (ushort*)takef(16 * SZ);
+    a.Gs   = (ushort*)takef(16 * SZ);
+    a.As   = (ushort*)takef(16 * SZ);
+    a.Us   = (ushort*)takef(16 * SZ);
+    float* ATsF = takef(48 * SZ);
+    a.ATs  = (ushort*)ATsF;
+    a.PVs  = (ushort*)takef(3 * SZ);
+    a.KQTs = (ushort*)takef(3 * SZ);
+    a.KQs  = (ushort*)takef(3 * SZ);
+    a.Ps   = (ushort*)takef(3 * SZ);
+    a.WqTs = (ushort*)takef(3 * SZ);
+    a.WkTs = (ushort*)takef(3 * SZ);
+    a.WvTs = (ushort*)takef(3 * SZ);
+    a.embs = (ushort*)takef(16384);
+    a.embTs= (ushort*)takef(16384);
+    a.q0f  = takef(RS);
+    a.q1s  = (ushort*)takef(16 * RS);
+    a.q2s  = (ushort*)takef(16 * RS);
+    a.LBs  = (ushort*)takef(16 * RS);
+    a.part = ATsF;
+
+    int mb = 0;
+    hipError_t qerr = hipOccupancyMaxActiveBlocksPerMultiprocessor(&mb, mega_k, 256, 0);
+    int grid = 256;
+    if (qerr == hipSuccess && mb >= 1) {
+        int m = mb > 4 ? 4 : mb;
+        grid = 256 * m;
+        if (grid > 1024) grid = 1024;
+    }
+
+    void* kp[] = { &a };
+    hipError_t err = hipLaunchCooperativeKernel(mega_k, dim3(grid), dim3(256),
+                                                kp, 0, stream);
+    if (err != hipSuccess) {
+        static const int cnt[17] = {1367,240,385,400,800,1200,400,800,1200,400,
+                                    400,400,160,160,160,160,1024};
+        for (int s = 0; s < 17; ++s)
+            stage_k<<<cnt[s], 256, 0, stream>>>(a, s);
+    }
+}
```

Measured after the change: 1.192 ms. 278% more time.
